# Kernel optimization log

Hardware: AMD Instinct MI355X
Metric: run time of the kernel (lower is better)

The kernel has to match this reference:

```python
import jax, jax.numpy as jnp
import numpy as np


def setup_inputs() -> dict:
    key = jax.random.key(0)
    k0, k1, k2 = jax.random.split(key, 3)
    B, S, H, D = 2, 2048, 16, 128  # flash-attn layout [batch, seq, heads, head_dim]
    q = jax.random.normal(k0, (B, S, H, D), dtype=jnp.float32)
    k = jax.random.normal(k1, (B, S, H, D), dtype=jnp.float32)
    v = jax.random.normal(k2, (B, S, H, D), dtype=jnp.float32)
    return {"_in0": q, "_in1": k, "_in2": v}


def reference(_in0, _in1, _in2):
    # Ring attention computes exact (non-causal, default) scaled dot-product
    # attention over the full sequence; the ring KV rotation is a distributed
    # execution detail, not a change in math. Single-device math:
    q, k, v = _in0, _in1, _in2
    D = q.shape[-1]
    scale = 1.0 / jnp.sqrt(jnp.asarray(D, dtype=q.dtype))
    # scores: [B, H, Sq, Sk]
    scores = jnp.einsum("bqhd,bkhd->bhqk", q, k) * scale
    probs = jax.nn.softmax(scores, axis=-1)
    out = jnp.einsum("bhqk,bkhd->bqhd", probs, v)
    return out
```

## Files before the change

### kernel.cpp

```cpp
#include <hip/hip_runtime.h>
#include <hip/hip_bf16.h>

typedef __attribute__((ext_vector_type(8))) short short8;
typedef __attribute__((ext_vector_type(16))) float f32x16;
typedef __attribute__((ext_vector_type(4))) unsigned int uint4v;

#define NB 2
#define NS 2048
#define NH 16
#define ND 128
#define ROWS (NH * ND)
#define KVBLK 64
#define QBLK 256
#define NTILE (NS / KVBLK)
#define NQB (NS / QBLK)
#define NWIN (NTILE / 2)
#define TILEB 16384

__device__ __forceinline__ unsigned short f2bf(float f) {
  union { __hip_bfloat16 b; unsigned short u; } c;
  c.b = __float2bfloat16(f);
  return c.u;
}

__device__ __forceinline__ short8 pack8(float4 a, float4 b, float s) {
  short8 r;
  r[0] = (short)f2bf(a.x * s); r[1] = (short)f2bf(a.y * s);
  r[2] = (short)f2bf(a.z * s); r[3] = (short)f2bf(a.w * s);
  r[4] = (short)f2bf(b.x * s); r[5] = (short)f2bf(b.y * s);
  r[6] = (short)f2bf(b.z * s); r[7] = (short)f2bf(b.w * s);
  return r;
}

__device__ __forceinline__ void dma16(const void* g, void* l) {
  __builtin_amdgcn_global_load_lds(
      (const __attribute__((address_space(1))) unsigned int*)g,
      (__attribute__((address_space(3))) unsigned int*)l, 16, 0, 0);
}

__device__ __forceinline__ void pl32swap(unsigned int& a, unsigned int& b) {
  asm("v_permlane32_swap_b32 %0, %1" : "+v"(a), "+v"(b));
}

__device__ __forceinline__ float fexp2(float x) {
  return __builtin_amdgcn_exp2f(x);
}

__global__ __launch_bounds__(256) void prepass_kv(
    const float* __restrict__ Kg, const float* __restrict__ Vg,
    char* __restrict__ Kimg, char* __restrict__ Vimg) {
  const int blk = blockIdx.x;
  const int t = blk & (NTILE - 1);
  const int bh = blk >> 5;
  const int h = bh & (NH - 1);
  const int b = bh >> 4;
  const int tid = threadIdx.x;

  const size_t ibase = (size_t)b * NS * ROWS + (size_t)h * ND + (size_t)t * KVBLK * ROWS;
  const float* Kp = Kg + ibase;
  const float* Vp = Vg + ibase;
  char* Kt = Kimg + (size_t)blk * TILEB;
  char* Vt = Vimg + (size_t)blk * TILEB;

  __shared__ float st[64][129];

#pragma unroll
  for (int j = 0; j < 4; ++j) {
    const int r = j * 16 + (tid >> 4);
    const int c0 = (tid & 15) * 8;
    float4 a = *reinterpret_cast<const float4*>(Kp + (size_t)r * ROWS + c0);
    float4 d = *reinterpret_cast<const float4*>(Kp + (size_t)r * ROWS + c0 + 4);
    st[r][c0 + 0] = a.x; st[r][c0 + 1] = a.y; st[r][c0 + 2] = a.z; st[r][c0 + 3] = a.w;
    st[r][c0 + 4] = d.x; st[r][c0 + 5] = d.y; st[r][c0 + 6] = d.z; st[r][c0 + 7] = d.w;
  }
  __syncthreads();
#pragma unroll
  for (int it = 0; it < 4; ++it) {
    const int item = it * 256 + tid;
    const int g = item >> 6;
    const int ll = item & 63;
    const int row = (g >> 3) * 32 + (ll & 31);
    const int kc = (g & 7) * 16 + (ll >> 5) * 8;
    short8 o8;
#pragma unroll
    for (int e = 0; e < 8; ++e) o8[e] = (short)f2bf(st[row][kc + e]);
    *reinterpret_cast<short8*>(Kt + (g * 64 + ll) * 16) = o8;
  }
  __syncthreads();

#pragma unroll
  for (int j = 0; j < 4; ++j) {
    const int r = j * 16 + (tid >> 4);
    const int c0 = (tid & 15) * 8;
    float4 a = *reinterpret_cast<const float4*>(Vp + (size_t)r * ROWS + c0);
    float4 d = *reinterpret_cast<const float4*>(Vp + (size_t)r * ROWS + c0 + 4);
    st[r][c0 + 0] = a.x; st[r][c0 + 1] = a.y; st[r][c0 + 2] = a.z; st[r][c0 + 3] = a.w;
    st[r][c0 + 4] = d.x; st[r][c0 + 5] = d.y; st[r][c0 + 6] = d.z; st[r][c0 + 7] = d.w;
  }
  __syncthreads();
#pragma unroll
  for (int it = 0; it < 4; ++it) {
    const int item = it * 256 + tid;
    const int g = item >> 6;
    const int ll = item & 63;
    const int d = (g >> 2) * 32 + (ll & 31);
    const int kv = (g & 3) * 16 + (ll >> 5) * 8;
    short8 o8;
#pragma unroll
    for (int e = 0; e < 8; ++e) o8[e] = (short)f2bf(st[kv + e][d]);
    *reinterpret_cast<short8*>(Vt + (g * 64 + ll) * 16) = o8;
  }
}

__global__ __launch_bounds__(512, 2) void fattn_fwd(
    const float* __restrict__ Qg, const char* __restrict__ Kimg,
    const char* __restrict__ Vimg, float* __restrict__ Og) {
  __shared__ __align__(16) char lds[131072];
  const int tid = threadIdx.x;
  const int l = tid & 63;
  const int w = tid >> 6;
  const int l31 = l & 31;
  const int hi2 = l >> 5;
  const int lo16 = l * 16;

  const int orig = blockIdx.x;
  const int wg = (orig & 7) * 32 + (orig >> 3);
  const int qblk = wg & (NQB - 1);
  const int bh = wg >> 3;
  const int h = bh & (NH - 1);
  const int b = bh >> 4;

  const float* Qp = Qg + (size_t)b * NS * ROWS + (size_t)h * ND;
  float* Op = Og + (size_t)b * NS * ROWS + (size_t)h * ND;
  const char* Ktiles = Kimg + (size_t)bh * NTILE * TILEB;
  const char* Vtiles = Vimg + (size_t)bh * NTILE * TILEB;

  const float scale = 0.08838834764831845f * 1.4426950408889634f;

  const int qrow = qblk * QBLK + w * 32 + l31;
  short8 qf[8];
  {
    const float* qr = Qp + (size_t)qrow * ROWS + hi2 * 8;
#pragma unroll
    for (int ks = 0; ks < 8; ++ks) {
      float4 a = *reinterpret_cast<const float4*>(qr + ks * 16);
      float4 c = *reinterpret_cast<const float4*>(qr + ks * 16 + 4);
      qf[ks] = pack8(a, c, scale);
    }
  }

  auto stageT = [&](int t, int s) {
    const char* Ks = Ktiles + (size_t)t * TILEB;
    const char* Vs = Vtiles + (size_t)t * TILEB;
    char* kd = lds + s * 32768;
    char* vd = kd + 16384;
#pragma unroll
    for (int i = 0; i < 2; ++i) {
      const int off = i * 8192 + w * 1024;
      dma16(Ks + off + lo16, kd + off);
      dma16(Vs + off + lo16, vd + off);
    }
  };

  f32x16 o[4];
#pragma unroll
  for (int dt = 0; dt < 4; ++dt) o[dt] = 0.f;
  float l_acc = 0.f;

  auto qkc = [&](const char* kb, int mtbase) -> f32x16 {
    f32x16 a = 0.f;
#pragma unroll
    for (int ks = 0; ks < 8; ++ks) {
      short8 kf = *reinterpret_cast<const short8*>(kb + lo16 + (mtbase + ks) * 1024);
      a = __builtin_amdgcn_mfma_f32_32x32x16_bf16(kf, qf[ks], a, 0, 0, 0);
    }
    return a;
  };

  auto sm = [&](const f32x16& acc, short8& f0, short8& f1) {
    f32x16 p;
#pragma unroll
    for (int r = 0; r < 16; ++r) p[r] = fexp2(acc[r]);
    float s01 = (p[0] + p[1]) + (p[2] + p[3]);
    float s23 = (p[4] + p[5]) + (p[6] + p[7]);
    float s45 = (p[8] + p[9]) + (p[10] + p[11]);
    float s67 = (p[12] + p[13]) + (p[14] + p[15]);
    l_acc += (s01 + s23) + (s45 + s67);
    unsigned int X[4];
#pragma unroll
    for (int j = 0; j < 4; ++j)
      X[j] = (unsigned int)f2bf(p[2 * j]) | ((unsigned int)f2bf(p[2 * j + 1]) << 16);
    pl32swap(X[0], X[2]);
    pl32swap(X[1], X[3]);
    uint4v u0 = {X[0], X[1], X[2], X[3]};
    f0 = __builtin_bit_cast(short8, u0);
    unsigned int Y[4];
#pragma unroll
    for (int j = 0; j < 4; ++j)
      Y[j] = (unsigned int)f2bf(p[8 + 2 * j]) | ((unsigned int)f2bf(p[8 + 2 * j + 1]) << 16);
    pl32swap(Y[0], Y[2]);
    pl32swap(Y[1], Y[3]);
    uint4v u1 = {Y[0], Y[1], Y[2], Y[3]};
    f1 = __builtin_bit_cast(short8, u1);
  };

  auto pvh = [&](const char* vb, int ks0, short8 f0, short8 f1) {
#pragma unroll
    for (int dt = 0; dt < 4; ++dt) {
      short8 v0 = *reinterpret_cast<const short8*>(vb + lo16 + (dt * 4 + ks0) * 1024);
      o[dt] = __builtin_amdgcn_mfma_f32_32x32x16_bf16(v0, f0, o[dt], 0, 0, 0);
      short8 v1 = *reinterpret_cast<const short8*>(vb + lo16 + (dt * 4 + ks0 + 1) * 1024);
      o[dt] = __builtin_amdgcn_mfma_f32_32x32x16_bf16(v1, f1, o[dt], 0, 0, 0);
    }
  };

  stageT(0, 0);
  stageT(1, 1);
  asm volatile("s_waitcnt vmcnt(0)" ::: "memory");
  __syncthreads();

#pragma unroll 1
  for (int j = 0; j < NWIN; ++j) {
    if (j + 1 < NWIN) {
      const int s0 = ((j & 1) ^ 1) * 2;
      stageT(2 * j + 2, s0);
      stageT(2 * j + 3, s0 + 1);
    }
    const char* kb0 = lds + (j & 1) * 65536;
    const char* kb1 = kb0 + 32768;
    const char* vb0 = kb0 + 16384;
    const char* vb1 = kb1 + 16384;

    f32x16 a0 = qkc(kb0, 0);
    f32x16 a1 = qkc(kb0, 8);
    f32x16 a2 = qkc(kb1, 0);
    f32x16 a3 = qkc(kb1, 8);
    short8 p00, p01, p10, p11;
    sm(a0, p00, p01);
    sm(a1, p10, p11);
    pvh(vb0, 0, p00, p01);
    pvh(vb0, 2, p10, p11);
    short8 p20, p21, p30, p31;
    sm(a2, p20, p21);
    sm(a3, p30, p31);
    pvh(vb1, 0, p20, p21);
    pvh(vb1, 2, p30, p31);

    if (j + 1 < NWIN) {
      asm volatile("s_waitcnt vmcnt(0)" ::: "memory");
      __syncthreads();
    }
  }

  const float lt = l_acc + __shfl_xor(l_acc, 32);
  const float inv = 1.0f / lt;
  float* orow = Op + (size_t)qrow * ROWS;
#pragma unroll
  for (int dt = 0; dt < 4; ++dt) {
#pragma unroll
    for (int g = 0; g < 4; ++g) {
      float4 v;
      v.x = o[dt][g * 4 + 0] * inv;
      v.y = o[dt][g * 4 + 1] * inv;
      v.z = o[dt][g * 4 + 2] * inv;
      v.w = o[dt][g * 4 + 3] * inv;
      *reinterpret_cast<float4*>(orow + dt * 32 + g * 8 + hi2 * 4) = v;
    }
  }
}

extern "C" void kernel_launch(void* const* d_in, const int* in_sizes, int n_in,
                              void* d_out, int out_size, void* d_ws, size_t ws_size,
                              hipStream_t stream) {
  const float* q = (const float*)d_in[0];
  const float* k = (const float*)d_in[1];
  const float* v = (const float*)d_in[2];
  float* out = (float*)d_out;
  (void)in_sizes; (void)n_in; (void)out_size; (void)ws_size;
  char* Kimg = (char*)d_ws;
  char* Vimg = Kimg + (size_t)NB * NH * NTILE * TILEB;
  prepass_kv<<<dim3(NB * NH * NTILE), dim3(256), 0, stream>>>(k, v, Kimg, Vimg);
  fattn_fwd<<<dim3(NQB * NB * NH), dim3(512), 0, stream>>>(q, Kimg, Vimg, out);
}
```

Measured before the change: 97.43 us.

## Give each wave two 32-row query tiles and halve the workgroup size

```diff
diff --git a/kernel.cpp b/kernel.cpp
--- a/kernel.cpp
+++ b/kernel.cpp
@@ -112,7 +112,7 @@
   }
 }
 
-__global__ __launch_bounds__(512, 2) void fattn_fwd(
+__global__ __launch_bounds__(256, 1) void fattn_fwd(
     const float* __restrict__ Qg, const char* __restrict__ Kimg,
     const char* __restrict__ Vimg, float* __restrict__ Og) {
   __shared__ __align__(16) char lds[131072];
@@ -137,15 +137,19 @@
 
   const float scale = 0.08838834764831845f * 1.4426950408889634f;
 
-  const int qrow = qblk * QBLK + w * 32 + l31;
-  short8 qf[8];
+  const int qrow0 = qblk * QBLK + w * 64 + l31;
+  short8 qf0[8], qf1[8];
   {
-    const float* qr = Qp + (size_t)qrow * ROWS + hi2 * 8;
+    const float* qr0 = Qp + (size_t)qrow0 * ROWS + hi2 * 8;
+    const float* qr1 = qr0 + (size_t)32 * ROWS;
 #pragma unroll
     for (int ks = 0; ks < 8; ++ks) {
-      float4 a = *reinterpret_cast<const float4*>(qr + ks * 16);
-      float4 c = *reinterpret_cast<const float4*>(qr + ks * 16 + 4);
-      qf[ks] = pack8(a, c, scale);
+      float4 a = *reinterpret_cast<const float4*>(qr0 + ks * 16);
+      float4 c = *reinterpret_cast<const float4*>(qr0 + ks * 16 + 4);
+      qf0[ks] = pack8(a, c, scale);
+      float4 d = *reinterpret_cast<const float4*>(qr1 + ks * 16);
+      float4 e = *reinterpret_cast<const float4*>(qr1 + ks * 16 + 4);
+      qf1[ks] = pack8(d, e, scale);
     }
   }
 
@@ -155,29 +159,22 @@
     char* kd = lds + s * 32768;
     char* vd = kd + 16384;
 #pragma unroll
-    for (int i = 0; i < 2; ++i) {
-      const int off = i * 8192 + w * 1024;
+    for (int i = 0; i < 4; ++i) {
+      const int off = i * 4096 + w * 1024;
       dma16(Ks + off + lo16, kd + off);
       dma16(Vs + off + lo16, vd + off);
     }
   };
 
-  f32x16 o[4];
-#pragma unroll
-  for (int dt = 0; dt < 4; ++dt) o[dt] = 0.f;
-  float l_acc = 0.f;
-
-  auto qkc = [&](const char* kb, int mtbase) -> f32x16 {
-    f32x16 a = 0.f;
-#pragma unroll
-    for (int ks = 0; ks < 8; ++ks) {
-      short8 kf = *reinterpret_cast<const short8*>(kb + lo16 + (mtbase + ks) * 1024);
-      a = __builtin_amdgcn_mfma_f32_32x32x16_bf16(kf, qf[ks], a, 0, 0, 0);
-    }
-    return a;
-  };
-
-  auto sm = [&](const f32x16& acc, short8& f0, short8& f1) {
+  f32x16 o[4][2];
+#pragma unroll
+  for (int dt = 0; dt < 4; ++dt) {
+    o[dt][0] = 0.f;
+    o[dt][1] = 0.f;
+  }
+  float lac0 = 0.f, lac1 = 0.f;
+
+  auto sm = [&](const f32x16& acc, short8& f0, short8& f1, float& lac) {
     f32x16 p;
 #pragma unroll
     for (int r = 0; r < 16; ++r) p[r] = fexp2(acc[r]);
@@ -185,7 +182,7 @@
     float s23 = (p[4] + p[5]) + (p[6] + p[7]);
     float s45 = (p[8] + p[9]) + (p[10] + p[11]);
     float s67 = (p[12] + p[13]) + (p[14] + p[15]);
-    l_acc += (s01 + s23) + (s45 + s67);
+    lac += (s01 + s23) + (s45 + s67);
     unsigned int X[4];
 #pragma unroll
     for (int j = 0; j < 4; ++j)
@@ -204,13 +201,29 @@
     f1 = __builtin_bit_cast(short8, u1);
   };
 
-  auto pvh = [&](const char* vb, int ks0, short8 f0, short8 f1) {
+  auto qk = [&](const char* kb, f32x16 A[2][2]) {
+#pragma unroll
+    for (int mt = 0; mt < 2; ++mt) {
+      A[mt][0] = 0.f;
+      A[mt][1] = 0.f;
+#pragma unroll
+      for (int ks = 0; ks < 8; ++ks) {
+        short8 kf = *reinterpret_cast<const short8*>(kb + lo16 + (mt * 8 + ks) * 1024);
+        A[mt][0] = __builtin_amdgcn_mfma_f32_32x32x16_bf16(kf, qf0[ks], A[mt][0], 0, 0, 0);
+        A[mt][1] = __builtin_amdgcn_mfma_f32_32x32x16_bf16(kf, qf1[ks], A[mt][1], 0, 0, 0);
+      }
+    }
+  };
+
+  auto pv = [&](const char* vb, const short8 pf[4][2]) {
 #pragma unroll
     for (int dt = 0; dt < 4; ++dt) {
-      short8 v0 = *reinterpret_cast<const short8*>(vb + lo16 + (dt * 4 + ks0) * 1024);
-      o[dt] = __builtin_amdgcn_mfma_f32_32x32x16_bf16(v0, f0, o[dt], 0, 0, 0);
-      short8 v1 = *reinterpret_cast<const short8*>(vb + lo16 + (dt * 4 + ks0 + 1) * 1024);
-      o[dt] = __builtin_amdgcn_mfma_f32_32x32x16_bf16(v1, f1, o[dt], 0, 0, 0);
+#pragma unroll
+      for (int ksl = 0; ksl < 4; ++ksl) {
+        short8 vf = *reinterpret_cast<const short8*>(vb + lo16 + (dt * 4 + ksl) * 1024);
+        o[dt][0] = __builtin_amdgcn_mfma_f32_32x32x16_bf16(vf, pf[ksl][0], o[dt][0], 0, 0, 0);
+        o[dt][1] = __builtin_amdgcn_mfma_f32_32x32x16_bf16(vf, pf[ksl][1], o[dt][1], 0, 0, 0);
+      }
     }
   };
 
@@ -231,20 +244,22 @@
     const char* vb0 = kb0 + 16384;
     const char* vb1 = kb1 + 16384;
 
-    f32x16 a0 = qkc(kb0, 0);
-    f32x16 a1 = qkc(kb0, 8);
-    f32x16 a2 = qkc(kb1, 0);
-    f32x16 a3 = qkc(kb1, 8);
-    short8 p00, p01, p10, p11;
-    sm(a0, p00, p01);
-    sm(a1, p10, p11);
-    pvh(vb0, 0, p00, p01);
-    pvh(vb0, 2, p10, p11);
-    short8 p20, p21, p30, p31;
-    sm(a2, p20, p21);
-    sm(a3, p30, p31);
-    pvh(vb1, 0, p20, p21);
-    pvh(vb1, 2, p30, p31);
+    f32x16 A0[2][2];
+    qk(kb0, A0);
+    f32x16 A1[2][2];
+    qk(kb1, A1);
+    short8 pf[4][2];
+    sm(A0[0][0], pf[0][0], pf[1][0], lac0);
+    sm(A0[0][1], pf[0][1], pf[1][1], lac1);
+    sm(A0[1][0], pf[2][0], pf[3][0], lac0);
+    sm(A0[1][1], pf[2][1], pf[3][1], lac1);
+    pv(vb0, pf);
+    short8 pg[4][2];
+    sm(A1[0][0], pg[0][0], pg[1][0], lac0);
+    sm(A1[0][1], pg[0][1], pg[1][1], lac1);
+    sm(A1[1][0], pg[2][0], pg[3][0], lac0);
+    sm(A1[1][1], pg[2][1], pg[3][1], lac1);
+    pv(vb1, pg);
 
     if (j + 1 < NWIN) {
       asm volatile("s_waitcnt vmcnt(0)" ::: "memory");
@@ -252,19 +267,23 @@
     }
   }
 
-  const float lt = l_acc + __shfl_xor(l_acc, 32);
-  const float inv = 1.0f / lt;
-  float* orow = Op + (size_t)qrow * ROWS;
-#pragma unroll
-  for (int dt = 0; dt < 4; ++dt) {
-#pragma unroll
-    for (int g = 0; g < 4; ++g) {
-      float4 v;
-      v.x = o[dt][g * 4 + 0] * inv;
-      v.y = o[dt][g * 4 + 1] * inv;
-      v.z = o[dt][g * 4 + 2] * inv;
-      v.w = o[dt][g * 4 + 3] * inv;
-      *reinterpret_cast<float4*>(orow + dt * 32 + g * 8 + hi2 * 4) = v;
+  const float lt0 = lac0 + __shfl_xor(lac0, 32);
+  const float lt1 = lac1 + __shfl_xor(lac1, 32);
+#pragma unroll
+  for (int qh = 0; qh < 2; ++qh) {
+    const float inv = 1.0f / (qh ? lt1 : lt0);
+    float* orow = Op + (size_t)(qrow0 + qh * 32) * ROWS;
+#pragma unroll
+    for (int dt = 0; dt < 4; ++dt) {
+#pragma unroll
+      for (int g = 0; g < 4; ++g) {
+        float4 v;
+        v.x = o[dt][qh][g * 4 + 0] * inv;
+        v.y = o[dt][qh][g * 4 + 1] * inv;
+        v.z = o[dt][qh][g * 4 + 2] * inv;
+        v.w = o[dt][qh][g * 4 + 3] * inv;
+        *reinterpret_cast<float4*>(orow + dt * 32 + g * 8 + hi2 * 4) = v;
+      }
     }
   }
 }
@@ -280,5 +299,5 @@
   char* Kimg = (char*)d_ws;
   char* Vimg = Kimg + (size_t)NB * NH * NTILE * TILEB;
   prepass_kv<<<dim3(NB * NH * NTILE), dim3(256), 0, stream>>>(k, v, Kimg, Vimg);
-  fattn_fwd<<<dim3(NQB * NB * NH), dim3(512), 0, stream>>>(q, Kimg, Vimg, out);
-}
+  fattn_fwd<<<dim3(NQB * NB * NH), dim3(256), 0, stream>>>(q, Kimg, Vimg, out);
+}
```

Measured after the change: 110.4 us. 1.13x slower.
